# Optimization experiments

Measured on AMD Instinct MI355X. Metric: run time of the kernel, lower is better.

## Reference

```python
import jax, jax.numpy as jnp
import numpy as np

N = 50000
E = 600000
NFEAT = 128
NHID = 128
PAD_N = 60000


def setup_inputs() -> dict:
    key = jax.random.key(0)
    ks = jax.random.split(key, 10)
    x = jax.random.normal(ks[0], (N, NFEAT), dtype=jnp.float32)
    edge_index = jax.random.randint(ks[1], (2, E), 0, N, dtype=jnp.int64)
    pos_idx = jnp.arange(N, dtype=jnp.int64)
    # SAGEConv params: lin_l (applied to mean-aggregated neighbors, with bias),
    # lin_r (applied to root/self features, no bias). Two layers.
    s1 = 1.0 / np.sqrt(NFEAT)
    s2 = 1.0 / np.sqrt(NHID)
    Wl1 = jax.random.uniform(ks[2], (NFEAT, NHID), jnp.float32, -s1, s1)
    Wr1 = jax.random.uniform(ks[3], (NFEAT, NHID), jnp.float32, -s1, s1)
    b1 = jax.random.uniform(ks[4], (NHID,), jnp.float32, -s1, s1)
    Wl2 = jax.random.uniform(ks[5], (NHID, NHID), jnp.float32, -s2, s2)
    Wr2 = jax.random.uniform(ks[6], (NHID, NHID), jnp.float32, -s2, s2)
    b2 = jax.random.uniform(ks[7], (NHID,), jnp.float32, -s2, s2)
    return {"x": x, "edge_index": edge_index, "pos_idx": pos_idx, "pad_n": PAD_N,
            "Wl1": Wl1, "Wr1": Wr1, "b1": b1, "Wl2": Wl2, "Wr2": Wr2, "b2": b2}


def _sage_conv(h, src, dst, Wl, Wr, b):
    # mean aggregation of source features into destination nodes
    msg = h[src]                                              # [E, F]
    agg = jax.ops.segment_sum(msg, dst, num_segments=N)       # [N, F]
    cnt = jax.ops.segment_sum(jnp.ones((dst.shape[0],), h.dtype), dst, num_segments=N)
    agg = agg / jnp.maximum(cnt, 1.0)[:, None]
    return agg @ Wl + h @ Wr + b


def reference(x, edge_index, pos_idx, pad_n, Wl1, Wr1, b1, Wl2, Wr2, b2):
    src, dst = edge_index[0], edge_index[1]
    h = jax.nn.relu(_sage_conv(x, src, dst, Wl1, Wr1, b1))
    # dropout is a no-op in eval mode (training=False)
    h = jax.nn.relu(_sage_conv(h, src, dst, Wl2, Wr2, b2))
    out = jnp.zeros((pad_n, h.shape[1]), h.dtype).at[pos_idx].set(h)
    return out
```

## Files before the change

### kernel.cpp

```cpp
#include <hip/hip_runtime.h>


#define NF 128
#define CAP 64

typedef _Float16 f16x8 __attribute__((ext_vector_type(8)));
typedef _Float16 f16x4 __attribute__((ext_vector_type(4)));
typedef float f32x4 __attribute__((ext_vector_type(4)));

__device__ __forceinline__ void swizzle_w(const float* __restrict__ Wl,
                                          const float* __restrict__ Wr,
                                          _Float16* __restrict__ Wf, int t) {
    int lane = t & 63;
    int frag = t >> 6;
    int s = frag >> 3, c = frag & 7;
    int n = s * 16 + (lane & 15);
    int kbase = c * 32 + (lane >> 4) * 8;
    f16x8 v;
#pragma unroll
    for (int j = 0; j < 8; ++j) {
        int k = kbase + j;
        float f = (k < NF) ? Wl[k * NF + n] : Wr[(k - NF) * NF + n];
        v[j] = (_Float16)f;
    }
    ((f16x8*)Wf)[frag * 64 + lane] = v;
}

__global__ void mega_prep_kernel(const int* __restrict__ src, const int* __restrict__ dst,
                                 int* __restrict__ deg, int* __restrict__ csr, int E,
                                 const float4* __restrict__ x4, f16x4* __restrict__ xh4,
                                 int n4x,
                                 float4* __restrict__ tail, int n4tail,
                                 const float* __restrict__ Wl1, const float* __restrict__ Wr1,
                                 _Float16* __restrict__ Wf1,
                                 const float* __restrict__ Wl2, const float* __restrict__ Wr2,
                                 _Float16* __restrict__ Wf2) {
    int nbe = (E + 255) >> 8;
    int nbc = (n4x + 255) >> 8;
    int nbt = (n4tail + 255) >> 8;
    int b = blockIdx.x;
    if (b < nbe) {
        int e = b * 256 + threadIdx.x;
        if (e < E) {
            int s = src[e];
            int d = dst[e];
            int slot = atomicAdd(&deg[d], 1);
            if (slot < CAP) __builtin_nontemporal_store(s, &csr[d * CAP + slot]);
        }
    } else if (b < nbe + nbc) {
        int i = (b - nbe) * 256 + threadIdx.x;
        if (i < n4x) {
            float4 v = x4[i];
            f16x4 o;
            o[0] = (_Float16)v.x; o[1] = (_Float16)v.y;
            o[2] = (_Float16)v.z; o[3] = (_Float16)v.w;
            xh4[i] = o;
        }
    } else if (b < nbe + nbc + nbt) {
        int i = (b - nbe - nbc) * 256 + threadIdx.x;
        if (i < n4tail) tail[i] = make_float4(0.f, 0.f, 0.f, 0.f);
    } else if (b < nbe + nbc + nbt + 16) {
        swizzle_w(Wl1, Wr1, Wf1, (b - nbe - nbc - nbt) * 256 + threadIdx.x);
    } else {
        swizzle_w(Wl2, Wr2, Wf2, (b - nbe - nbc - nbt - 16) * 256 + threadIdx.x);
    }
}

#define LDA 136
template <bool LAST>
__global__ __launch_bounds__(256) void sage_layer_fused(
    const int* __restrict__ csr, const int* __restrict__ deg,
    const _Float16* __restrict__ H,
    const _Float16* __restrict__ Wf,
    const float* __restrict__ bias,
    const int* __restrict__ pos,
    _Float16* __restrict__ outh,
    float* __restrict__ outf,
    int Nn) {
    __shared__ _Float16 sA[16][LDA];

    const int wave = threadIdx.x >> 6;
    const int lane = threadIdx.x & 63;
    const int sub  = lane >> 4;
    const int li   = lane & 15;
    const int m0 = blockIdx.x * 16;

    {
        int n = m0 + wave * 4 + sub;
        float a[8] = {0.f, 0.f, 0.f, 0.f, 0.f, 0.f, 0.f, 0.f};
        float b[8] = {0.f, 0.f, 0.f, 0.f, 0.f, 0.f, 0.f, 0.f};
        float inv = 1.0f;
        if (n < Nn) {
            int dg = deg[n];
            int rs = n * CAP;
            int re = rs + ((dg < CAP) ? dg : CAP);
            const f16x8* Hp = (const f16x8*)H;
            int k = rs;
            for (; k + 4 <= re; k += 4) {
                f16x8 v0 = Hp[(size_t)csr[k] * 16 + li];
                f16x8 v1 = Hp[(size_t)csr[k + 1] * 16 + li];
                f16x8 v2 = Hp[(size_t)csr[k + 2] * 16 + li];
                f16x8 v3 = Hp[(size_t)csr[k + 3] * 16 + li];
#pragma unroll
                for (int j = 0; j < 8; ++j) {
                    a[j] += (float)v0[j] + (float)v2[j];
                    b[j] += (float)v1[j] + (float)v3[j];
                }
            }
            if (k + 2 <= re) {
                f16x8 v0 = Hp[(size_t)csr[k] * 16 + li];
                f16x8 v1 = Hp[(size_t)csr[k + 1] * 16 + li];
#pragma unroll
                for (int j = 0; j < 8; ++j) { a[j] += (float)v0[j]; b[j] += (float)v1[j]; }
                k += 2;
            }
            if (k < re) {
                f16x8 v0 = Hp[(size_t)csr[k] * 16 + li];
#pragma unroll
                for (int j = 0; j < 8; ++j) a[j] += (float)v0[j];
            }
            inv = 1.0f / fmaxf((float)dg, 1.0f);
        }
        f16x8 r;
#pragma unroll
        for (int j = 0; j < 8; ++j) r[j] = (_Float16)((a[j] + b[j]) * inv);
        *(f16x8*)&sA[wave * 4 + sub][li * 8] = r;
    }

    f16x8 bfrag[2][8];
    const f16x8* wfp = (const f16x8*)Wf;
#pragma unroll
    for (int s = 0; s < 2; ++s)
#pragma unroll
        for (int c = 0; c < 8; ++c)
            bfrag[s][c] = wfp[((2 * wave + s) * 8 + c) * 64 + lane];

    __syncthreads();

    f32x4 acc[2] = {(f32x4){0.f, 0.f, 0.f, 0.f}, (f32x4){0.f, 0.f, 0.f, 0.f}};

#pragma unroll
    for (int c = 0; c < 4; ++c) {
        f16x8 af = *(const f16x8*)&sA[li][c * 32 + sub * 8];
        acc[0] = __builtin_amdgcn_mfma_f32_16x16x32_f16(af, bfrag[0][c], acc[0], 0, 0, 0);
        acc[1] = __builtin_amdgcn_mfma_f32_16x16x32_f16(af, bfrag[1][c], acc[1], 0, 0, 0);
    }
    {
        int nd = m0 + li; if (nd >= Nn) nd = Nn - 1;
        const _Float16* xrow = H + (size_t)nd * NF;
#pragma unroll
        for (int c = 0; c < 4; ++c) {
            f16x8 af = *(const f16x8*)(xrow + c * 32 + sub * 8);
            acc[0] = __builtin_amdgcn_mfma_f32_16x16x32_f16(af, bfrag[0][4 + c], acc[0], 0, 0, 0);
            acc[1] = __builtin_amdgcn_mfma_f32_16x16x32_f16(af, bfrag[1][4 + c], acc[1], 0, 0, 0);
        }
    }

#pragma unroll
    for (int s = 0; s < 2; ++s) {
        int feat = (2 * wave + s) * 16 + li;
        float bv = bias[feat];
#pragma unroll
        for (int r = 0; r < 4; ++r) {
            int node = m0 + sub * 4 + r;
            if (node < Nn) {
                float v = fmaxf(acc[s][r] + bv, 0.f);
                if (LAST) outf[(size_t)pos[node] * NF + feat] = v;
                else      outh[(size_t)node * NF + feat] = (_Float16)v;
            }
        }
    }
}

extern "C" void kernel_launch(void* const* d_in, const int* in_sizes, int n_in,
                              void* d_out, int out_size, void* d_ws, size_t ws_size,
                              hipStream_t stream) {
    const float* x   = (const float*)d_in[0];
    const int*   ei  = (const int*)d_in[1];
    const int*   pos = (const int*)d_in[2];
    const float* Wl1 = (const float*)d_in[4];
    const float* Wr1 = (const float*)d_in[5];
    const float* b1  = (const float*)d_in[6];
    const float* Wl2 = (const float*)d_in[7];
    const float* Wr2 = (const float*)d_in[8];
    const float* b2  = (const float*)d_in[9];
    float* out = (float*)d_out;

    const int Nn = in_sizes[0] / NF;
    const int E  = in_sizes[1] / 2;
    const int* src = ei;
    const int* dst = ei + E;
    const int pad_rows = out_size / NF;

    const int degN = (Nn + 3) & ~3;
    _Float16* xh   = (_Float16*)d_ws;
    _Float16* h1h  = xh + (size_t)Nn * NF;
    _Float16* Wf1  = h1h + (size_t)Nn * NF;
    _Float16* Wf2  = Wf1 + 64 * 64 * 8;
    int* deg       = (int*)(Wf2 + 64 * 64 * 8);
    int* csr       = deg + degN;

    const int ZB = 256;

    hipMemsetAsync(deg, 0, (size_t)degN * sizeof(int), stream);

    int n4x = Nn * NF / 4;
    int n4tail = (pad_rows - Nn) * NF / 4;
    int nbe = (E + ZB - 1) / ZB;
    int nbc = (n4x + ZB - 1) / ZB;
    int nbt = (n4tail + ZB - 1) / ZB;
    mega_prep_kernel<<<nbe + nbc + nbt + 32, ZB, 0, stream>>>(
        src, dst, deg, csr, E,
        (const float4*)x, (f16x4*)xh, n4x,
        (float4*)(out + (size_t)Nn * NF), n4tail,
        Wl1, Wr1, Wf1, Wl2, Wr2, Wf2);

    const int fblocks = (Nn + 15) / 16;
    sage_layer_fused<false><<<fblocks, ZB, 0, stream>>>(
        csr, deg, xh, Wf1, b1, nullptr, h1h, nullptr, Nn);
    sage_layer_fused<true><<<fblocks, ZB, 0, stream>>>(
        csr, deg, h1h, Wf2, b2, pos, nullptr, out, Nn);
}
```

Baseline: 213.6 us.

## Use persistent grid-stride tiles and pad degree counters to reduce atomic contention

The fused SAGE layer kernels become persistent. A fixed grid of 1042 blocks strides over 16-node tiles, loading the weight fragments and biases once per block instead of once per tile. A double-buffered shared tile replaces the single buffer, so only one barrier is needed per iteration. The degree counters are also padded to a 16-int stride (64 bytes) so that concurrent atomics on neighbouring nodes land on separate cache lines. In exchange, the memset grows sixteenfold and the degree reads become strided, so each gather loses locality on deg.

```diff
diff --git a/kernel.cpp b/kernel.cpp
--- a/kernel.cpp
+++ b/kernel.cpp
@@ -3,6 +3,9 @@
 
 #define NF 128
 #define CAP 64
+#define DSTR 16
+#define LDA 136
+#define GSB 1042
 
 typedef _Float16 f16x8 __attribute__((ext_vector_type(8)));
 typedef _Float16 f16x4 __attribute__((ext_vector_type(4)));
@@ -44,7 +47,7 @@
         if (e < E) {
             int s = src[e];
             int d = dst[e];
-            int slot = atomicAdd(&deg[d], 1);
+            int slot = atomicAdd(&deg[d * DSTR], 1);
             if (slot < CAP) __builtin_nontemporal_store(s, &csr[d * CAP + slot]);
         }
     } else if (b < nbe + nbc) {
@@ -66,7 +69,6 @@
     }
 }
 
-#define LDA 136
 template <bool LAST>
 __global__ __launch_bounds__(256) void sage_layer_fused(
     const int* __restrict__ csr, const int* __restrict__ deg,
@@ -76,56 +78,13 @@
     const int* __restrict__ pos,
     _Float16* __restrict__ outh,
     float* __restrict__ outf,
-    int Nn) {
-    __shared__ _Float16 sA[16][LDA];
+    int Nn, int ntiles) {
+    __shared__ _Float16 sA[2][16][LDA];
 
     const int wave = threadIdx.x >> 6;
     const int lane = threadIdx.x & 63;
     const int sub  = lane >> 4;
     const int li   = lane & 15;
-    const int m0 = blockIdx.x * 16;
-
-    {
-        int n = m0 + wave * 4 + sub;
-        float a[8] = {0.f, 0.f, 0.f, 0.f, 0.f, 0.f, 0.f, 0.f};
-        float b[8] = {0.f, 0.f, 0.f, 0.f, 0.f, 0.f, 0.f, 0.f};
-        float inv = 1.0f;
-        if (n < Nn) {
-            int dg = deg[n];
-            int rs = n * CAP;
-            int re = rs + ((dg < CAP) ? dg : CAP);
-            const f16x8* Hp = (const f16x8*)H;
-            int k = rs;
-            for (; k + 4 <= re; k += 4) {
-                f16x8 v0 = Hp[(size_t)csr[k] * 16 + li];
-                f16x8 v1 = Hp[(size_t)csr[k + 1] * 16 + li];
-                f16x8 v2 = Hp[(size_t)csr[k + 2] * 16 + li];
-                f16x8 v3 = Hp[(size_t)csr[k + 3] * 16 + li];
-#pragma unroll
-                for (int j = 0; j < 8; ++j) {
-                    a[j] += (float)v0[j] + (float)v2[j];
-                    b[j] += (float)v1[j] + (float)v3[j];
-                }
-            }
-            if (k + 2 <= re) {
-                f16x8 v0 = Hp[(size_t)csr[k] * 16 + li];
-                f16x8 v1 = Hp[(size_t)csr[k + 1] * 16 + li];
-#pragma unroll
-                for (int j = 0; j < 8; ++j) { a[j] += (float)v0[j]; b[j] += (float)v1[j]; }
-                k += 2;
-            }
-            if (k < re) {
-                f16x8 v0 = Hp[(size_t)csr[k] * 16 + li];
-#pragma unroll
-                for (int j = 0; j < 8; ++j) a[j] += (float)v0[j];
-            }
-            inv = 1.0f / fmaxf((float)dg, 1.0f);
-        }
-        f16x8 r;
-#pragma unroll
-        for (int j = 0; j < 8; ++j) r[j] = (_Float16)((a[j] + b[j]) * inv);
-        *(f16x8*)&sA[wave * 4 + sub][li * 8] = r;
-    }
 
     f16x8 bfrag[2][8];
     const f16x8* wfp = (const f16x8*)Wf;
@@ -135,38 +94,88 @@
         for (int c = 0; c < 8; ++c)
             bfrag[s][c] = wfp[((2 * wave + s) * 8 + c) * 64 + lane];
 
-    __syncthreads();
-
-    f32x4 acc[2] = {(f32x4){0.f, 0.f, 0.f, 0.f}, (f32x4){0.f, 0.f, 0.f, 0.f}};
-
-#pragma unroll
-    for (int c = 0; c < 4; ++c) {
-        f16x8 af = *(const f16x8*)&sA[li][c * 32 + sub * 8];
-        acc[0] = __builtin_amdgcn_mfma_f32_16x16x32_f16(af, bfrag[0][c], acc[0], 0, 0, 0);
-        acc[1] = __builtin_amdgcn_mfma_f32_16x16x32_f16(af, bfrag[1][c], acc[1], 0, 0, 0);
-    }
-    {
-        int nd = m0 + li; if (nd >= Nn) nd = Nn - 1;
-        const _Float16* xrow = H + (size_t)nd * NF;
+    const float bv0 = bias[(2 * wave + 0) * 16 + li];
+    const float bv1 = bias[(2 * wave + 1) * 16 + li];
+
+    int buf = 0;
+    for (int tile = blockIdx.x; tile < ntiles; tile += gridDim.x, buf ^= 1) {
+        const int m0 = tile * 16;
+
+        {
+            int n = m0 + wave * 4 + sub;
+            float a[8] = {0.f, 0.f, 0.f, 0.f, 0.f, 0.f, 0.f, 0.f};
+            float b[8] = {0.f, 0.f, 0.f, 0.f, 0.f, 0.f, 0.f, 0.f};
+            float inv = 1.0f;
+            if (n < Nn) {
+                int dg = deg[n * DSTR];
+                int rs = n * CAP;
+                int re = rs + ((dg < CAP) ? dg : CAP);
+                const f16x8* Hp = (const f16x8*)H;
+                int k = rs;
+                for (; k + 4 <= re; k += 4) {
+                    f16x8 v0 = Hp[(size_t)csr[k] * 16 + li];
+                    f16x8 v1 = Hp[(size_t)csr[k + 1] * 16 + li];
+                    f16x8 v2 = Hp[(size_t)csr[k + 2] * 16 + li];
+                    f16x8 v3 = Hp[(size_t)csr[k + 3] * 16 + li];
+#pragma unroll
+                    for (int j = 0; j < 8; ++j) {
+                        a[j] += (float)v0[j] + (float)v2[j];
+                        b[j] += (float)v1[j] + (float)v3[j];
+                    }
+                }
+                if (k + 2 <= re) {
+                    f16x8 v0 = Hp[(size_t)csr[k] * 16 + li];
+                    f16x8 v1 = Hp[(size_t)csr[k + 1] * 16 + li];
+#pragma unroll
+                    for (int j = 0; j < 8; ++j) { a[j] += (float)v0[j]; b[j] += (float)v1[j]; }
+                    k += 2;
+                }
+                if (k < re) {
+                    f16x8 v0 = Hp[(size_t)csr[k] * 16 + li];
+#pragma unroll
+                    for (int j = 0; j < 8; ++j) a[j] += (float)v0[j];
+                }
+                inv = 1.0f / fmaxf((float)dg, 1.0f);
+            }
+            f16x8 r;
+#pragma unroll
+            for (int j = 0; j < 8; ++j) r[j] = (_Float16)((a[j] + b[j]) * inv);
+            *(f16x8*)&sA[buf][wave * 4 + sub][li * 8] = r;
+        }
+
+        __syncthreads();
+
+        f32x4 acc[2] = {(f32x4){0.f, 0.f, 0.f, 0.f}, (f32x4){0.f, 0.f, 0.f, 0.f}};
+
 #pragma unroll
         for (int c = 0; c < 4; ++c) {
-            f16x8 af = *(const f16x8*)(xrow + c * 32 + sub * 8);
-            acc[0] = __builtin_amdgcn_mfma_f32_16x16x32_f16(af, bfrag[0][4 + c], acc[0], 0, 0, 0);
-            acc[1] = __builtin_amdgcn_mfma_f32_16x16x32_f16(af, bfrag[1][4 + c], acc[1], 0, 0, 0);
-        }
-    }
-
-#pragma unroll
-    for (int s = 0; s < 2; ++s) {
-        int feat = (2 * wave + s) * 16 + li;
-        float bv = bias[feat];
-#pragma unroll
-        for (int r = 0; r < 4; ++r) {
-            int node = m0 + sub * 4 + r;
-            if (node < Nn) {
-                float v = fmaxf(acc[s][r] + bv, 0.f);
-                if (LAST) outf[(size_t)pos[node] * NF + feat] = v;
-                else      outh[(size_t)node * NF + feat] = (_Float16)v;
+            f16x8 af = *(const f16x8*)&sA[buf][li][c * 32 + sub * 8];
+            acc[0] = __builtin_amdgcn_mfma_f32_16x16x32_f16(af, bfrag[0][c], acc[0], 0, 0, 0);
+            acc[1] = __builtin_amdgcn_mfma_f32_16x16x32_f16(af, bfrag[1][c], acc[1], 0, 0, 0);
+        }
+        {
+            int nd = m0 + li; if (nd >= Nn) nd = Nn - 1;
+            const _Float16* xrow = H + (size_t)nd * NF;
+#pragma unroll
+            for (int c = 0; c < 4; ++c) {
+                f16x8 af = *(const f16x8*)(xrow + c * 32 + sub * 8);
+                acc[0] = __builtin_amdgcn_mfma_f32_16x16x32_f16(af, bfrag[0][4 + c], acc[0], 0, 0, 0);
+                acc[1] = __builtin_amdgcn_mfma_f32_16x16x32_f16(af, bfrag[1][4 + c], acc[1], 0, 0, 0);
+            }
+        }
+
+#pragma unroll
+        for (int s = 0; s < 2; ++s) {
+            int feat = (2 * wave + s) * 16 + li;
+            float bv = s ? bv1 : bv0;
+#pragma unroll
+            for (int r = 0; r < 4; ++r) {
+                int node = m0 + sub * 4 + r;
+                if (node < Nn) {
+                    float v = fmaxf(acc[s][r] + bv, 0.f);
+                    if (LAST) outf[(size_t)pos[node] * NF + feat] = v;
+                    else      outh[(size_t)node * NF + feat] = (_Float16)v;
+                }
             }
         }
     }
@@ -192,17 +201,16 @@
     const int* dst = ei + E;
     const int pad_rows = out_size / NF;
 
-    const int degN = (Nn + 3) & ~3;
     _Float16* xh   = (_Float16*)d_ws;
     _Float16* h1h  = xh + (size_t)Nn * NF;
     _Float16* Wf1  = h1h + (size_t)Nn * NF;
     _Float16* Wf2  = Wf1 + 64 * 64 * 8;
     int* deg       = (int*)(Wf2 + 64 * 64 * 8);
-    int* csr       = deg + degN;
+    int* csr       = deg + (size_t)Nn * DSTR;
 
     const int ZB = 256;
 
-    hipMemsetAsync(deg, 0, (size_t)degN * sizeof(int), stream);
+    hipMemsetAsync(deg, 0, (size_t)Nn * DSTR * sizeof(int), stream);
 
     int n4x = Nn * NF / 4;
     int n4tail = (pad_rows - Nn) * NF / 4;
@@ -215,9 +223,9 @@
         (float4*)(out + (size_t)Nn * NF), n4tail,
         Wl1, Wr1, Wf1, Wl2, Wr2, Wf2);
 
-    const int fblocks = (Nn + 15) / 16;
-    sage_layer_fused<false><<<fblocks, ZB, 0, stream>>>(
-        csr, deg, xh, Wf1, b1, nullptr, h1h, nullptr, Nn);
-    sage_layer_fused<true><<<fblocks, ZB, 0, stream>>>(
-        csr, deg, h1h, Wf2, b2, pos, nullptr, out, Nn);
-}
+    const int ntiles = (Nn + 15) / 16;
+    sage_layer_fused<false><<<GSB, ZB, 0, stream>>>(
+        csr, deg, xh, Wf1, b1, nullptr, h1h, nullptr, Nn, ntiles);
+    sage_layer_fused<true><<<GSB, ZB, 0, stream>>>(
+        csr, deg, h1h, Wf2, b2, pos, nullptr, out, Nn, ntiles);
+}
```

Measured after the change: 230.6 us. 1.08x slower.
